# Kernel optimization log

Hardware: AMD Instinct MI355X
Metric: run time of the kernel (lower is better)

## Reference

```python
import jax, jax.numpy as jnp
import numpy as np

B, T, D, P = 32, 2048, 256, 100000
MAX_SPAN = 16


def setup_inputs() -> dict:
    key = jax.random.key(0)
    k0, k1, k2, k3, k4, k5 = jax.random.split(key, 6)
    token_embs = jax.random.normal(k0, (B, T, D), dtype=jnp.float32)
    p1_span = jax.random.randint(k1, (P,), 1, MAX_SPAN + 1, dtype=jnp.int32)
    p2_span = jax.random.randint(k2, (P,), 1, MAX_SPAN + 1, dtype=jnp.int32)
    p1_start = jax.random.randint(k3, (P,), 0, T - MAX_SPAN, dtype=jnp.int32)
    p2_start = jax.random.randint(k4, (P,), 0, T - MAX_SPAN, dtype=jnp.int32)
    pair_batch = jax.random.randint(k5, (P,), 0, B, dtype=jnp.int32)
    return {
        "token_embs": token_embs,
        "p1_start": p1_start,
        "p1_span": p1_span,
        "p2_start": p2_start,
        "p2_span": p2_span,
        "pair_batch": pair_batch,
    }


def reference(token_embs, p1_start, p1_span, p2_start, p2_span, pair_batch):
    # token_embs: [B, T, D]; per-pair ranges [start, start+span) within batch row pair_batch.
    # Range mean via exclusive prefix sums: mean = (csum[end] - csum[start]) / span.
    b, t, d = token_embs.shape
    csum = jnp.concatenate(
        [jnp.zeros((b, 1, d), token_embs.dtype), jnp.cumsum(token_embs, axis=1)],
        axis=1,
    )  # [B, T+1, D]

    def span_mean(start, span):
        end = start + span
        s = csum[pair_batch, end] - csum[pair_batch, start]  # [P, D]
        return s / span[:, None].astype(token_embs.dtype)

    p1 = span_mean(p1_start, p1_span)
    p2 = span_mean(p2_start, p2_span)
    return jnp.concatenate([p1, p2], axis=-1)  # [P, 2D]
```

## Files before the change

kernel.cpp:

```cpp
#include <hip/hip_runtime.h>


#define PB_B 32
#define PB_T 2048
#define PB_TP1 2049
#define PB_D 256
#define PB_P 100000
#define CHUNK 64
#define NCHUNK (PB_T / CHUNK)

__global__ __launch_bounds__(256) void chunk_sum_kernel(
    const float* __restrict__ emb, float* __restrict__ cs)
{
    const int wid  = blockIdx.x * 4 + (threadIdx.x >> 6);
    const int lane = threadIdx.x & 63;
    const int b = wid >> 5;
    const int c = wid & (NCHUNK - 1);

    const float4* __restrict__ src =
        (const float4*)(emb + ((long long)b * PB_T + c * CHUNK) * PB_D) + lane;
    float4 acc = make_float4(0.f, 0.f, 0.f, 0.f);
    #pragma unroll 8
    for (int t = 0; t < CHUNK; ++t) {
        float4 v = src[t * (PB_D / 4)];
        acc.x += v.x; acc.y += v.y; acc.z += v.z; acc.w += v.w;
    }
    ((float4*)(cs + ((long long)b * NCHUNK + c) * PB_D))[lane] = acc;
}

__global__ __launch_bounds__(256) void chunk_scan_kernel(float* __restrict__ cs)
{
    const int b = blockIdx.x;
    const int d = threadIdx.x;
    float run = 0.f;
    #pragma unroll
    for (int c = 0; c < NCHUNK; ++c) {
        float* p = cs + ((long long)b * NCHUNK + c) * PB_D + d;
        float v = *p;
        *p = run;
        run += v;
    }
}

__global__ __launch_bounds__(256) void csum_write_kernel(
    const float* __restrict__ emb, const float* __restrict__ cs,
    float* __restrict__ csum)
{
    const int wid  = blockIdx.x * 4 + (threadIdx.x >> 6);
    const int lane = threadIdx.x & 63;
    const int b = wid >> 5;
    const int c = wid & (NCHUNK - 1);

    float4 acc = ((const float4*)(cs + ((long long)b * NCHUNK + c) * PB_D))[lane];
    const float4* __restrict__ src =
        (const float4*)(emb + ((long long)b * PB_T + c * CHUNK) * PB_D) + lane;
    float4* __restrict__ dst =
        (float4*)(csum + ((long long)b * PB_TP1 + c * CHUNK + 1) * PB_D) + lane;

    if (c == 0) {
        ((float4*)(csum + (long long)b * PB_TP1 * PB_D))[lane] =
            make_float4(0.f, 0.f, 0.f, 0.f);
    }
    #pragma unroll 8
    for (int t = 0; t < CHUNK; ++t) {
        float4 v = src[t * (PB_D / 4)];
        acc.x += v.x; acc.y += v.y; acc.z += v.z; acc.w += v.w;
        dst[t * (PB_D / 4)] = acc;
    }
}

__global__ __launch_bounds__(256) void hist_kernel(
    const int* __restrict__ pair_batch, int* __restrict__ counts)
{
    __shared__ int l_cnt[PB_B];
    if (threadIdx.x < PB_B) l_cnt[threadIdx.x] = 0;
    __syncthreads();
    const int i = blockIdx.x * 256 + threadIdx.x;
    if (i < PB_P) atomicAdd(&l_cnt[pair_batch[i]], 1);
    __syncthreads();
    if (threadIdx.x < PB_B && l_cnt[threadIdx.x] > 0)
        atomicAdd(&counts[threadIdx.x], l_cnt[threadIdx.x]);
}

__global__ void scan_counts_kernel(const int* __restrict__ counts,
                                   int* __restrict__ cursors)
{
    if (threadIdx.x == 0 && blockIdx.x == 0) {
        int run = 0;
        #pragma unroll
        for (int b = 0; b < PB_B; ++b) { cursors[b] = run; run += counts[b]; }
    }
}

__global__ __launch_bounds__(256) void scatter_kernel(
    const int* __restrict__ pair_batch, int* __restrict__ cursors,
    int* __restrict__ perm)
{
    __shared__ int l_cnt[PB_B];
    __shared__ int l_base[PB_B];
    if (threadIdx.x < PB_B) l_cnt[threadIdx.x] = 0;
    __syncthreads();
    const int i = blockIdx.x * 256 + threadIdx.x;
    int b = 0, lpos = 0;
    const bool valid = (i < PB_P);
    if (valid) { b = pair_batch[i]; lpos = atomicAdd(&l_cnt[b], 1); }
    __syncthreads();
    if (threadIdx.x < PB_B && l_cnt[threadIdx.x] > 0)
        l_base[threadIdx.x] = atomicAdd(&cursors[threadIdx.x], l_cnt[threadIdx.x]);
    __syncthreads();
    if (valid) perm[l_base[b] + lpos] = i;
}

__global__ __launch_bounds__(256) void gather_kernel(
    const float* __restrict__ csum, const int* __restrict__ perm,
    const int* __restrict__ p1_start, const int* __restrict__ p1_span,
    const int* __restrict__ p2_start, const int* __restrict__ p2_span,
    const int* __restrict__ pair_batch,
    float* __restrict__ out)
{
    const int pos_block = (blockIdx.x & 7) * (25000 / 8) + (blockIdx.x >> 3);
    const int pos = pos_block * 4 + (threadIdx.x >> 6);
    const int lane = threadIdx.x & 63;

    const int pair = perm[pos];
    const int b  = pair_batch[pair];
    const int s1 = p1_start[pair], n1 = p1_span[pair];
    const int s2 = p2_start[pair], n2 = p2_span[pair];

    const float* base = csum + (long long)b * PB_TP1 * PB_D;
    float4 e1 = ((const float4*)(base + (long long)(s1 + n1) * PB_D))[lane];
    float4 b1 = ((const float4*)(base + (long long)s1 * PB_D))[lane];
    float4 e2 = ((const float4*)(base + (long long)(s2 + n2) * PB_D))[lane];
    float4 b2 = ((const float4*)(base + (long long)s2 * PB_D))[lane];

    const float i1 = 1.f / (float)n1;
    const float i2 = 1.f / (float)n2;
    float4 r1 = make_float4((e1.x - b1.x) * i1, (e1.y - b1.y) * i1,
                            (e1.z - b1.z) * i1, (e1.w - b1.w) * i1);
    float4 r2 = make_float4((e2.x - b2.x) * i2, (e2.y - b2.y) * i2,
                            (e2.z - b2.z) * i2, (e2.w - b2.w) * i2);

    float4* o = (float4*)(out + (long long)pair * (2 * PB_D));
    o[lane]      = r1;
    o[64 + lane] = r2;
}

extern "C" void kernel_launch(void* const* d_in, const int* in_sizes, int n_in,
                              void* d_out, int out_size, void* d_ws, size_t ws_size,
                              hipStream_t stream) {
    const float* token_embs = (const float*)d_in[0];
    const int* p1_start = (const int*)d_in[1];
    const int* p1_span  = (const int*)d_in[2];
    const int* p2_start = (const int*)d_in[3];
    const int* p2_span  = (const int*)d_in[4];
    const int* pair_batch = (const int*)d_in[5];
    float* out = (float*)d_out;

    const size_t csum_elems = (size_t)PB_B * PB_TP1 * PB_D;
    const size_t cs_elems   = (size_t)PB_B * NCHUNK * PB_D;

    float* csum = (float*)d_ws;
    float* cs   = csum + csum_elems;
    int* counts  = (int*)(cs + cs_elems);
    int* cursors = counts + PB_B;
    int* perm    = cursors + PB_B;

    const int nwave_bc = PB_B * NCHUNK;
    chunk_sum_kernel<<<nwave_bc / 4, 256, 0, stream>>>(token_embs, cs);
    chunk_scan_kernel<<<PB_B, 256, 0, stream>>>(cs);
    csum_write_kernel<<<nwave_bc / 4, 256, 0, stream>>>(token_embs, cs, csum);

    hipMemsetAsync(counts, 0, PB_B * sizeof(int), stream);
    const int hb = (PB_P + 255) / 256;
    hist_kernel<<<hb, 256, 0, stream>>>(pair_batch, counts);
    scan_counts_kernel<<<1, 64, 0, stream>>>(counts, cursors);
    scatter_kernel<<<hb, 256, 0, stream>>>(pair_batch, cursors, perm);

    gather_kernel<<<PB_P / 4, 256, 0, stream>>>(
        csum, perm, p1_start, p1_span, p2_start, p2_span, pair_batch, out);
}
```

Before: 338.7 us.

## Replace prefix-sum pipeline with direct span summation from embeddings

```diff
diff --git a/kernel.cpp b/kernel.cpp
--- a/kernel.cpp
+++ b/kernel.cpp
@@ -3,71 +3,10 @@
 
 #define PB_B 32
 #define PB_T 2048
-#define PB_TP1 2049
 #define PB_D 256
 #define PB_P 100000
-#define CHUNK 64
-#define NCHUNK (PB_T / CHUNK)
 
-__global__ __launch_bounds__(256) void chunk_sum_kernel(
-    const float* __restrict__ emb, float* __restrict__ cs)
-{
-    const int wid  = blockIdx.x * 4 + (threadIdx.x >> 6);
-    const int lane = threadIdx.x & 63;
-    const int b = wid >> 5;
-    const int c = wid & (NCHUNK - 1);
-
-    const float4* __restrict__ src =
-        (const float4*)(emb + ((long long)b * PB_T + c * CHUNK) * PB_D) + lane;
-    float4 acc = make_float4(0.f, 0.f, 0.f, 0.f);
-    #pragma unroll 8
-    for (int t = 0; t < CHUNK; ++t) {
-        float4 v = src[t * (PB_D / 4)];
-        acc.x += v.x; acc.y += v.y; acc.z += v.z; acc.w += v.w;
-    }
-    ((float4*)(cs + ((long long)b * NCHUNK + c) * PB_D))[lane] = acc;
-}
-
-__global__ __launch_bounds__(256) void chunk_scan_kernel(float* __restrict__ cs)
-{
-    const int b = blockIdx.x;
-    const int d = threadIdx.x;
-    float run = 0.f;
-    #pragma unroll
-    for (int c = 0; c < NCHUNK; ++c) {
-        float* p = cs + ((long long)b * NCHUNK + c) * PB_D + d;
-        float v = *p;
-        *p = run;
-        run += v;
-    }
-}
-
-__global__ __launch_bounds__(256) void csum_write_kernel(
-    const float* __restrict__ emb, const float* __restrict__ cs,
-    float* __restrict__ csum)
-{
-    const int wid  = blockIdx.x * 4 + (threadIdx.x >> 6);
-    const int lane = threadIdx.x & 63;
-    const int b = wid >> 5;
-    const int c = wid & (NCHUNK - 1);
-
-    float4 acc = ((const float4*)(cs + ((long long)b * NCHUNK + c) * PB_D))[lane];
-    const float4* __restrict__ src =
-        (const float4*)(emb + ((long long)b * PB_T + c * CHUNK) * PB_D) + lane;
-    float4* __restrict__ dst =
-        (float4*)(csum + ((long long)b * PB_TP1 + c * CHUNK + 1) * PB_D) + lane;
-
-    if (c == 0) {
-        ((float4*)(csum + (long long)b * PB_TP1 * PB_D))[lane] =
-            make_float4(0.f, 0.f, 0.f, 0.f);
-    }
-    #pragma unroll 8
-    for (int t = 0; t < CHUNK; ++t) {
-        float4 v = src[t * (PB_D / 4)];
-        acc.x += v.x; acc.y += v.y; acc.z += v.z; acc.w += v.w;
-        dst[t * (PB_D / 4)] = acc;
-    }
-}
+typedef float vfloat4 __attribute__((ext_vector_type(4)));
 
 __global__ __launch_bounds__(256) void hist_kernel(
     const int* __restrict__ pair_batch, int* __restrict__ counts)
@@ -93,8 +32,10 @@
 }
 
 __global__ __launch_bounds__(256) void scatter_kernel(
-    const int* __restrict__ pair_batch, int* __restrict__ cursors,
-    int* __restrict__ perm)
+    const int* __restrict__ pair_batch,
+    const int* __restrict__ p1_start, const int* __restrict__ p1_span,
+    const int* __restrict__ p2_start, const int* __restrict__ p2_span,
+    int* __restrict__ cursors, int4* __restrict__ meta)
 {
     __shared__ int l_cnt[PB_B];
     __shared__ int l_base[PB_B];
@@ -108,41 +49,55 @@
     if (threadIdx.x < PB_B && l_cnt[threadIdx.x] > 0)
         l_base[threadIdx.x] = atomicAdd(&cursors[threadIdx.x], l_cnt[threadIdx.x]);
     __syncthreads();
-    if (valid) perm[l_base[b] + lpos] = i;
+    if (valid) {
+        int4 m;
+        m.x = i;
+        m.y = p1_span[i] | (p2_span[i] << 8);
+        m.z = b * PB_T + p1_start[i];
+        m.w = b * PB_T + p2_start[i];
+        meta[l_base[b] + lpos] = m;
+    }
 }
 
 __global__ __launch_bounds__(256) void gather_kernel(
-    const float* __restrict__ csum, const int* __restrict__ perm,
-    const int* __restrict__ p1_start, const int* __restrict__ p1_span,
-    const int* __restrict__ p2_start, const int* __restrict__ p2_span,
-    const int* __restrict__ pair_batch,
+    const float* __restrict__ emb, const int4* __restrict__ meta,
     float* __restrict__ out)
 {
-    const int pos_block = (blockIdx.x & 7) * (25000 / 8) + (blockIdx.x >> 3);
-    const int pos = pos_block * 4 + (threadIdx.x >> 6);
+    const int pos_block = (blockIdx.x & 7) * (PB_P / 4 / 8) + (blockIdx.x >> 3);
+    const int pos  = pos_block * 4 + (threadIdx.x >> 6);
     const int lane = threadIdx.x & 63;
 
-    const int pair = perm[pos];
-    const int b  = pair_batch[pair];
-    const int s1 = p1_start[pair], n1 = p1_span[pair];
-    const int s2 = p2_start[pair], n2 = p2_span[pair];
+    const int4 m = meta[pos];
+    const int n1 = m.y & 0xff;
+    const int n2 = m.y >> 8;
 
-    const float* base = csum + (long long)b * PB_TP1 * PB_D;
-    float4 e1 = ((const float4*)(base + (long long)(s1 + n1) * PB_D))[lane];
-    float4 b1 = ((const float4*)(base + (long long)s1 * PB_D))[lane];
-    float4 e2 = ((const float4*)(base + (long long)(s2 + n2) * PB_D))[lane];
-    float4 b2 = ((const float4*)(base + (long long)s2 * PB_D))[lane];
+    const float4* __restrict__ r1 =
+        (const float4*)emb + (long long)m.z * (PB_D / 4) + lane;
+    const float4* __restrict__ r2 =
+        (const float4*)emb + (long long)m.w * (PB_D / 4) + lane;
+
+    float4 a1 = r1[0];
+    float4 a2 = r2[0];
+    const int nmax = (n1 > n2) ? n1 : n2;
+    for (int t = 1; t < nmax; ++t) {
+        if (t < n1) {
+            float4 v = r1[t * (PB_D / 4)];
+            a1.x += v.x; a1.y += v.y; a1.z += v.z; a1.w += v.w;
+        }
+        if (t < n2) {
+            float4 v = r2[t * (PB_D / 4)];
+            a2.x += v.x; a2.y += v.y; a2.z += v.z; a2.w += v.w;
+        }
+    }
 
     const float i1 = 1.f / (float)n1;
     const float i2 = 1.f / (float)n2;
-    float4 r1 = make_float4((e1.x - b1.x) * i1, (e1.y - b1.y) * i1,
-                            (e1.z - b1.z) * i1, (e1.w - b1.w) * i1);
-    float4 r2 = make_float4((e2.x - b2.x) * i2, (e2.y - b2.y) * i2,
-                            (e2.z - b2.z) * i2, (e2.w - b2.w) * i2);
+    vfloat4 o1 = { a1.x * i1, a1.y * i1, a1.z * i1, a1.w * i1 };
+    vfloat4 o2 = { a2.x * i2, a2.y * i2, a2.z * i2, a2.w * i2 };
 
-    float4* o = (float4*)(out + (long long)pair * (2 * PB_D));
-    o[lane]      = r1;
-    o[64 + lane] = r2;
+    vfloat4* o = (vfloat4*)(out + (long long)m.x * (2 * PB_D));
+    __builtin_nontemporal_store(o1, o + lane);
+    __builtin_nontemporal_store(o2, o + 64 + lane);
 }
 
 extern "C" void kernel_launch(void* const* d_in, const int* in_sizes, int n_in,
@@ -156,26 +111,16 @@
     const int* pair_batch = (const int*)d_in[5];
     float* out = (float*)d_out;
 
-    const size_t csum_elems = (size_t)PB_B * PB_TP1 * PB_D;
-    const size_t cs_elems   = (size_t)PB_B * NCHUNK * PB_D;
+    int4* meta   = (int4*)d_ws;
+    int* counts  = (int*)(meta + PB_P);
+    int* cursors = counts + PB_B;
 
-    float* csum = (float*)d_ws;
-    float* cs   = csum + csum_elems;
-    int* counts  = (int*)(cs + cs_elems);
-    int* cursors = counts + PB_B;
-    int* perm    = cursors + PB_B;
-
-    const int nwave_bc = PB_B * NCHUNK;
-    chunk_sum_kernel<<<nwave_bc / 4, 256, 0, stream>>>(token_embs, cs);
-    chunk_scan_kernel<<<PB_B, 256, 0, stream>>>(cs);
-    csum_write_kernel<<<nwave_bc / 4, 256, 0, stream>>>(token_embs, cs, csum);
-
-    hipMemsetAsync(counts, 0, PB_B * sizeof(int), stream);
+    (void)hipMemsetAsync(counts, 0, PB_B * sizeof(int), stream);
     const int hb = (PB_P + 255) / 256;
     hist_kernel<<<hb, 256, 0, stream>>>(pair_batch, counts);
     scan_counts_kernel<<<1, 64, 0, stream>>>(counts, cursors);
-    scatter_kernel<<<hb, 256, 0, stream>>>(pair_batch, cursors, perm);
+    scatter_kernel<<<hb, 256, 0, stream>>>(
+        pair_batch, p1_start, p1_span, p2_start, p2_span, cursors, meta);
 
-    gather_kernel<<<PB_P / 4, 256, 0, stream>>>(
-        csum, perm, p1_start, p1_span, p2_start, p2_span, pair_batch, out);
+    gather_kernel<<<PB_P / 4, 256, 0, stream>>>(token_embs, meta, out);
 }
```

Result: no change. 332.7 us (-1.8%).
